# Kernel tuning notes

Hardware: AMD Instinct MI355X
Metric: run time of the kernel (lower is better)

## Reference

```python
import jax, jax.numpy as jnp
import numpy as np

N = 256   # input_size
H = 512   # hidden_size
B = 128   # batch


def _make_masks(n, h):
    # Replicates MADE.create_masks with n_hidden=1
    d_in = np.arange(n)
    d_h = np.arange(h) % (n - 1)
    d_out = np.arange(n) % n - 1  # = arange(n) - 1
    m0 = (d_h[:, None] >= d_in[None, :]).astype(np.float32)   # (H, N)
    m1 = (d_h[:, None] >= d_h[None, :]).astype(np.float32)    # (H, H)
    m2 = (d_out[:, None] >= d_h[None, :]).astype(np.float32)  # (N, H)
    m2 = np.tile(m2, (2, 1))                                   # (2N, H)
    return jnp.asarray(m0), jnp.asarray(m1), jnp.asarray(m2)


def setup_inputs() -> dict:
    key = jax.random.key(0)
    ks = jax.random.split(key, 7)
    s = 0.02
    return {
        "z": jax.random.normal(ks[0], (B, N), jnp.float32),
        "w0": jax.random.normal(ks[1], (H, N), jnp.float32) * s,
        "b0": jax.random.normal(ks[2], (H,), jnp.float32) * s,
        "w1": jax.random.normal(ks[3], (H, H), jnp.float32) * s,
        "b1": jax.random.normal(ks[4], (H,), jnp.float32) * s,
        "w2": jax.random.normal(ks[5], (2 * N, H), jnp.float32) * s,
        "b2": jax.random.normal(ks[6], (2 * N,), jnp.float32) * s,
    }


def reference(z, w0, b0, w1, b1, w2, b2):
    m0, m1, m2 = _make_masks(N, H)
    mw0 = m0 * w0
    mw1 = m1 * w1
    mw2 = m2 * w2

    def net(x):
        h = jax.nn.relu(x @ mw0.T + b0)
        h = jax.nn.relu(h @ mw1.T + b1)
        return h @ mw2.T + b2  # (B, 2N)

    def step(carry, i):
        x, log_det = carry
        out = net(x)
        mu = out[:, i]          # (B,)
        alpha = out[:, N + i]   # (B,)
        x = x.at[:, i].set(mu + z[:, i] * jnp.exp(alpha))
        return (x, log_det + alpha), None

    x0 = jnp.zeros_like(z)
    ld0 = jnp.zeros((z.shape[0],), z.dtype)
    (x, log_det), _ = jax.lax.scan(step, (x0, ld0), jnp.arange(N))
    return x, -log_det
```

## Files before the change

### kernel.cpp

```cpp
#include <hip/hip_runtime.h>

#define NN 256
#define HH 512
#define BB 128
#define PKS (5 * HH)

typedef float f32x4 __attribute__((ext_vector_type(4)));

__global__ __launch_bounds__(512)
void made_prep(const float* __restrict__ w0,
               const float* __restrict__ w1,
               const float* __restrict__ w2,
               float* __restrict__ pk) {
    const int i = blockIdx.x;
    const int k = threadIdx.x;
    const int lev = k % 255;
    float* row = pk + (size_t)i * PKS;
    row[k]          = (lev < i)  ? w2[i * HH + k]        : 0.f;
    row[HH + k]     = (lev < i)  ? w2[(NN + i) * HH + k] : 0.f;
    row[2*HH + k]   = (lev >= i) ? w0[k * NN + i]        : 0.f;
    const int l1 = i % 255;
    row[3*HH + k]   = (lev >= l1) ? w1[k * HH + i]       : 0.f;
    const int j2 = i + 255;
    const int l2 = j2 % 255;
    row[4*HH + k]   = (lev >= l2) ? w1[k * HH + j2]      : 0.f;
}

struct B10 { f32x4 q0,q1,q2,q3,q4,q5,q6,q7,q8,q9; };

__device__ __forceinline__ float rl_f(float v, int lane) {
    return __int_as_float(__builtin_amdgcn_readlane(__float_as_int(v), lane));
}

__device__ __forceinline__ f32x4 ld4(const float* p) { return *(const f32x4*)p; }

__device__ __forceinline__ float q45c(const B10& b, int s) {
    switch (s) {
        case 0: return b.q4[0]; case 1: return b.q4[1];
        case 2: return b.q4[2]; case 3: return b.q4[3];
        case 4: return b.q5[0]; case 5: return b.q5[1];
        case 6: return b.q5[2]; default: return b.q5[3];
    }
}

#define DPP_ADD(v, ctrl, rm) \
    ((v) + __int_as_float(__builtin_amdgcn_update_dpp(0, __float_as_int(v), (ctrl), (rm), 0xf, false)))

__device__ __forceinline__ void reduce2(float& pm, float& pa) {
    pm = DPP_ADD(pm, 0x111, 0xf);  pa = DPP_ADD(pa, 0x111, 0xf);
    pm = DPP_ADD(pm, 0x112, 0xf);  pa = DPP_ADD(pa, 0x112, 0xf);
    pm = DPP_ADD(pm, 0x114, 0xf);  pa = DPP_ADD(pa, 0x114, 0xf);
    pm = DPP_ADD(pm, 0x118, 0xf);  pa = DPP_ADD(pa, 0x118, 0xf);
    pm = DPP_ADD(pm, 0x142, 0xa);  pa = DPP_ADD(pa, 0x142, 0xa);
    pm = DPP_ADD(pm, 0x143, 0xc);  pa = DPP_ADD(pa, 0x143, 0xc);
}

#define DOT8(res, A, B)  do {                                   \
    float t01_ = fmaf(h_[1], (A)[1], h_[0] * (A)[0]);           \
    float t23_ = fmaf(h_[3], (A)[3], h_[2] * (A)[2]);           \
    float t45_ = fmaf(h_[5], (B)[1], h_[4] * (B)[0]);           \
    float t67_ = fmaf(h_[7], (B)[3], h_[6] * (B)[2]);           \
    res = (t01_ + t23_) + (t45_ + t67_);                        \
} while (0)

#define STEP(g, r, BUF) do {                                                 \
    const int i_ = ((g) << 3) | (r);                                         \
    float h_[8];                                                             \
    h_[0] = fmaxf(a1v[0], 0.f); h_[1] = fmaxf(a1v[1], 0.f);                  \
    h_[2] = fmaxf(a1v[2], 0.f); h_[3] = fmaxf(a1v[3], 0.f);                  \
    h_[4] = fmaxf(a1v[4], 0.f); h_[5] = fmaxf(a1v[5], 0.f);                  \
    h_[6] = fmaxf(a1v[6], 0.f); h_[7] = fmaxf(a1v[7], 0.f);                  \
    float pm_, pa_;                                                          \
    DOT8(pa_, BUF.q2, BUF.q3);                                               \
    DOT8(pm_, BUF.q0, BUF.q1);                                               \
    reduce2(pm_, pa_);                                                       \
    const int sB_ = ((r) + 7) & 7;                                           \
    const int LB_ = ((r) == 0) ? ((g) + 31) : ((g) + 32);                    \
    const int zl_ = ((g) << 1) + ((r) >> 2);                                 \
    float a0A_ = rl_f(a0v[(r)], (g));                                        \
    float w0A_ = rl_f(q45c(BUF, (r)), (g));                                  \
    float a0B_ = rl_f(a0v[sB_], LB_);                                        \
    float w0B_ = rl_f(q45c(BUF, sB_), LB_);                                  \
    float ta_ = rl_f(pa_, 63), tm_ = rl_f(pm_, 63);                          \
    float al_ = ta_ + rl_f(b2v[(r)], (g) + 32);                              \
    float mu_ = tm_ + rl_f(b2v[(r)], (g));                                   \
    ldacc += al_;                                                            \
    float zi_ = rl_f(zrv[(r) & 3], zl_);                                     \
    float xi_ = fmaf(zi_, __expf(al_), mu_);                                 \
    xo[(r) & 3] = (t == zl_) ? xi_ : xo[(r) & 3];                            \
    float h0a_ = fmaxf(fmaf(xi_, w0A_, a0A_), 0.f);                          \
    float h0b_ = fmaxf(fmaf(xi_, w0B_, a0B_), 0.f);                          \
    if ((r) < 2 && (g) == 0) {          \
        float a0C_ = rl_f(a0v[6 + (r)], 63);                                 \
        float w0C_ = rl_f(q45c(BUF, 6 + (r)), 63);                           \
        float h0c_ = fmaxf(fmaf(xi_, w0C_, a0C_), 0.f);                      \
        const float* wc_ = ((r) == 0) ? w1c0v : w1c1v;                       \
        a1v[0] = fmaf(h0c_, wc_[0], a1v[0]); a1v[1] = fmaf(h0c_, wc_[1], a1v[1]); \
        a1v[2] = fmaf(h0c_, wc_[2], a1v[2]); a1v[3] = fmaf(h0c_, wc_[3], a1v[3]); \
        a1v[4] = fmaf(h0c_, wc_[4], a1v[4]); a1v[5] = fmaf(h0c_, wc_[5], a1v[5]); \
        a1v[6] = fmaf(h0c_, wc_[6], a1v[6]); a1v[7] = fmaf(h0c_, wc_[7], a1v[7]); \
    }                                                                        \
    a0v[0] = fmaf(xi_, BUF.q4[0], a0v[0]); a0v[1] = fmaf(xi_, BUF.q4[1], a0v[1]); \
    a0v[2] = fmaf(xi_, BUF.q4[2], a0v[2]); a0v[3] = fmaf(xi_, BUF.q4[3], a0v[3]); \
    a0v[4] = fmaf(xi_, BUF.q5[0], a0v[4]); a0v[5] = fmaf(xi_, BUF.q5[1], a0v[5]); \
    a0v[6] = fmaf(xi_, BUF.q5[2], a0v[6]); a0v[7] = fmaf(xi_, BUF.q5[3], a0v[7]); \
    a1v[0] = fmaf(h0b_, BUF.q8[0], fmaf(h0a_, BUF.q6[0], a1v[0]));           \
    a1v[1] = fmaf(h0b_, BUF.q8[1], fmaf(h0a_, BUF.q6[1], a1v[1]));           \
    a1v[2] = fmaf(h0b_, BUF.q8[2], fmaf(h0a_, BUF.q6[2], a1v[2]));           \
    a1v[3] = fmaf(h0b_, BUF.q8[3], fmaf(h0a_, BUF.q6[3], a1v[3]));           \
    a1v[4] = fmaf(h0b_, BUF.q9[0], fmaf(h0a_, BUF.q7[0], a1v[4]));           \
    a1v[5] = fmaf(h0b_, BUF.q9[1], fmaf(h0a_, BUF.q7[1], a1v[5]));           \
    a1v[6] = fmaf(h0b_, BUF.q9[2], fmaf(h0a_, BUF.q7[2], a1v[6]));           \
    a1v[7] = fmaf(h0b_, BUF.q9[3], fmaf(h0a_, BUF.q7[3], a1v[7]));           \
          \
    {                                                                        \
        const float* pf_ = pk + (size_t)((i_ + 4) & 255) * PKS + o8;         \
        BUF.q0 = ld4(pf_);          BUF.q1 = ld4(pf_ + 4);                   \
        BUF.q2 = ld4(pf_ + HH);     BUF.q3 = ld4(pf_ + HH + 4);              \
        BUF.q4 = ld4(pf_ + 2*HH);   BUF.q5 = ld4(pf_ + 2*HH + 4);            \
        BUF.q6 = ld4(pf_ + 3*HH);   BUF.q7 = ld4(pf_ + 3*HH + 4);            \
        BUF.q8 = ld4(pf_ + 4*HH);   BUF.q9 = ld4(pf_ + 4*HH + 4);            \
    }                                                                        \
    __builtin_amdgcn_sched_barrier(0);                                       \
} while (0)

__global__ __launch_bounds__(64, 1)
void made_seq64(const float* __restrict__ z,
                const float* __restrict__ b0g,
                const float* __restrict__ b1g,
                const float* __restrict__ b2g,
                const float* __restrict__ w1,
                const float* __restrict__ pk,
                float* __restrict__ out) {
    const int bb = blockIdx.x;
    const int t  = threadIdx.x;
    const int o8 = t << 3;

    float a0v[8], a1v[8], b2v[8];
    {
        f32x4 a = ld4(b0g + o8), b = ld4(b0g + o8 + 4);
        a0v[0]=a[0]; a0v[1]=a[1]; a0v[2]=a[2]; a0v[3]=a[3];
        a0v[4]=b[0]; a0v[5]=b[1]; a0v[6]=b[2]; a0v[7]=b[3];
        a = ld4(b1g + o8); b = ld4(b1g + o8 + 4);
        a1v[0]=a[0]; a1v[1]=a[1]; a1v[2]=a[2]; a1v[3]=a[3];
        a1v[4]=b[0]; a1v[5]=b[1]; a1v[6]=b[2]; a1v[7]=b[3];
        a = ld4(b2g + o8); b = ld4(b2g + o8 + 4);
        b2v[0]=a[0]; b2v[1]=a[1]; b2v[2]=a[2]; b2v[3]=a[3];
        b2v[4]=b[0]; b2v[5]=b[1]; b2v[6]=b[2]; b2v[7]=b[3];
    }
    float w1c0v[8], w1c1v[8];
    #pragma unroll
    for (int j = 0; j < 8; ++j) {
        const int k = o8 + j;
        w1c0v[j] = w1[k * HH + 510];
        w1c1v[j] = ((k % 255) >= 1) ? w1[k * HH + 511] : 0.f;
    }
    f32x4 z4 = ld4(z + (bb << 8) + (t << 2));
    float zrv[4] = {z4[0], z4[1], z4[2], z4[3]};
    float xo[4]  = {0.f, 0.f, 0.f, 0.f};
    float ldacc  = 0.f;

    B10 Ba, Bb, Bc, Bd;
    {
        const float* p0 = pk + o8;
        Ba.q0 = ld4(p0);        Ba.q1 = ld4(p0 + 4);
        Ba.q2 = ld4(p0 + HH);   Ba.q3 = ld4(p0 + HH + 4);
        Ba.q4 = ld4(p0 + 2*HH); Ba.q5 = ld4(p0 + 2*HH + 4);
        Ba.q6 = ld4(p0 + 3*HH); Ba.q7 = ld4(p0 + 3*HH + 4);
        Ba.q8 = ld4(p0 + 4*HH); Ba.q9 = ld4(p0 + 4*HH + 4);
        const float* p1 = pk + PKS + o8;
        Bb.q0 = ld4(p1);        Bb.q1 = ld4(p1 + 4);
        Bb.q2 = ld4(p1 + HH);   Bb.q3 = ld4(p1 + HH + 4);
        Bb.q4 = ld4(p1 + 2*HH); Bb.q5 = ld4(p1 + 2*HH + 4);
        Bb.q6 = ld4(p1 + 3*HH); Bb.q7 = ld4(p1 + 3*HH + 4);
        Bb.q8 = ld4(p1 + 4*HH); Bb.q9 = ld4(p1 + 4*HH + 4);
        const float* p2 = pk + 2*PKS + o8;
        Bc.q0 = ld4(p2);        Bc.q1 = ld4(p2 + 4);
        Bc.q2 = ld4(p2 + HH);   Bc.q3 = ld4(p2 + HH + 4);
        Bc.q4 = ld4(p2 + 2*HH); Bc.q5 = ld4(p2 + 2*HH + 4);
        Bc.q6 = ld4(p2 + 3*HH); Bc.q7 = ld4(p2 + 3*HH + 4);
        Bc.q8 = ld4(p2 + 4*HH); Bc.q9 = ld4(p2 + 4*HH + 4);
        const float* p3 = pk + 3*PKS + o8;
        Bd.q0 = ld4(p3);        Bd.q1 = ld4(p3 + 4);
        Bd.q2 = ld4(p3 + HH);   Bd.q3 = ld4(p3 + HH + 4);
        Bd.q4 = ld4(p3 + 2*HH); Bd.q5 = ld4(p3 + 2*HH + 4);
        Bd.q6 = ld4(p3 + 3*HH); Bd.q7 = ld4(p3 + 3*HH + 4);
        Bd.q8 = ld4(p3 + 4*HH); Bd.q9 = ld4(p3 + 4*HH + 4);
    }
    __builtin_amdgcn_sched_barrier(0);

    for (int g = 0; g < 32; ++g) {
        STEP(g, 0, Ba); STEP(g, 1, Bb); STEP(g, 2, Bc); STEP(g, 3, Bd);
        STEP(g, 4, Ba); STEP(g, 5, Bb); STEP(g, 6, Bc); STEP(g, 7, Bd);
    }

    *(f32x4*)(out + (bb << 8) + (t << 2)) = (f32x4){xo[0], xo[1], xo[2], xo[3]};
    if (t == 0) out[BB * NN + bb] = -ldacc;
}

__global__ __launch_bounds__(256)
void made_seq_fb(const float* __restrict__ z,
                 const float* __restrict__ w0, const float* __restrict__ b0,
                 const float* __restrict__ w1, const float* __restrict__ b1,
                 const float* __restrict__ w2, const float* __restrict__ b2,
                 float* __restrict__ out) {
    const int bb = blockIdx.x;
    const int t  = threadIdx.x;
    const int u0 = t, u1 = t + 256;
    const int l0 = u0 % 255, s0 = u0 / 255;
    const int l1 = u1 % 255, s1 = u1 / 255;
    const int wave = t >> 6, lane = t & 63;

    __shared__ float red[2][4][2];
    __shared__ float pub[2][3][2];

    float a0_0 = b0[u0], a0_1 = b0[u1];
    float a1_0 = b1[u0], a1_1 = b1[u1];
    float ld = 0.f;

    for (int i = 0; i < NN; ++i) {
        float cw2m0 = (l0 < i) ? w2[i * HH + u0] : 0.f;
        float cw2a0 = (l0 < i) ? w2[(NN + i) * HH + u0] : 0.f;
        float cw2m1 = (l1 < i) ? w2[i * HH + u1] : 0.f;
        float cw2a1 = (l1 < i) ? w2[(NN + i) * HH + u1] : 0.f;
        float cw00  = (l0 >= i) ? w0[u0 * NN + i] : 0.f;
        float cw01  = (l1 >= i) ? w0[u1 * NN + i] : 0.f;
        bool g0 = (l0 >= (i % 255)), g1 = (l1 >= (i % 255));
        float w1a0 = g0 ? w1[u0 * HH + i] : 0.f;
        float w1a1 = g1 ? w1[u1 * HH + i] : 0.f;
        float w1b0 = g0 ? w1[u0 * HH + i + 255] : 0.f;
        float w1b1 = g1 ? w1[u1 * HH + i + 255] : 0.f;

        float h10 = fmaxf(a1_0, 0.f), h11 = fmaxf(a1_1, 0.f);
        float pm = h10 * cw2m0 + h11 * cw2m1;
        float pa = h10 * cw2a0 + h11 * cw2a1;
        #pragma unroll
        for (int offs = 32; offs > 0; offs >>= 1) {
            pm += __shfl_xor(pm, offs);
            pa += __shfl_xor(pa, offs);
        }
        const int bf = i & 1;
        if (lane == 0) { red[bf][wave][0] = pm; red[bf][wave][1] = pa; }
        if (l0 == i) { pub[bf][s0][0] = a0_0; pub[bf][s0][1] = cw00; }
        if (l1 == i) { pub[bf][s1][0] = a0_1; pub[bf][s1][1] = cw01; }
        __syncthreads();

        float mu = b2[i]      + red[bf][0][0] + red[bf][1][0] + red[bf][2][0] + red[bf][3][0];
        float al = b2[NN + i] + red[bf][0][1] + red[bf][1][1] + red[bf][2][1] + red[bf][3][1];
        ld += al;
        float xi = fmaf(z[bb * NN + i], __expf(al), mu);
        if (t == 0) out[bb * NN + i] = xi;

        a0_0 = fmaf(xi, cw00, a0_0);
        a0_1 = fmaf(xi, cw01, a0_1);

        float h0a = fmaxf(fmaf(xi, pub[bf][0][1], pub[bf][0][0]), 0.f);
        float h0b = fmaxf(fmaf(xi, pub[bf][1][1], pub[bf][1][0]), 0.f);
        a1_0 = fmaf(h0a, w1a0, a1_0);
        a1_1 = fmaf(h0a, w1a1, a1_1);
        a1_0 = fmaf(h0b, w1b0, a1_0);
        a1_1 = fmaf(h0b, w1b1, a1_1);
        if (i < 2) {
            float w1c0 = (l0 >= i) ? w1[u0 * HH + i + 510] : 0.f;
            float w1c1 = (l1 >= i) ? w1[u1 * HH + i + 510] : 0.f;
            float h0c = fmaxf(fmaf(xi, pub[bf][2][1], pub[bf][2][0]), 0.f);
            a1_0 = fmaf(h0c, w1c0, a1_0);
            a1_1 = fmaf(h0c, w1c1, a1_1);
        }
        __syncthreads();
    }

    if (t == 0) out[BB * NN + bb] = -ld;
}

extern "C" void kernel_launch(void* const* d_in, const int* in_sizes, int n_in,
                              void* d_out, int out_size, void* d_ws, size_t ws_size,
                              hipStream_t stream) {
    const float* z  = (const float*)d_in[0];
    const float* w0 = (const float*)d_in[1];
    const float* b0 = (const float*)d_in[2];
    const float* w1 = (const float*)d_in[3];
    const float* b1 = (const float*)d_in[4];
    const float* w2 = (const float*)d_in[5];
    const float* b2 = (const float*)d_in[6];
    float* out = (float*)d_out;

    const size_t need = (size_t)NN * PKS * sizeof(float);
    if (ws_size >= need) {
        float* pk = (float*)d_ws;
        made_prep<<<NN, 512, 0, stream>>>(w0, w1, w2, pk);
        made_seq64<<<BB, 64, 0, stream>>>(z, b0, b1, b2, w1, pk, out);
    } else {
        made_seq_fb<<<BB, 256, 0, stream>>>(z, w0, b0, w1, b1, w2, b2, out);
    }
}
```

Before: 83.79 us.

## Process two batch rows per wavefront to reuse prefetched weight buffers

Each 64-lane block now handles two batch elements, so every weight tile loaded from the packed workspace feeds two dependency chains instead of one, and the grid is halved. The paired mu/alpha reduction is also restructured: a cross-half shuffle lets each half-wave reduce one quantity, which saves one DPP step. Interleaving two independent chains can hide the latency of the serial per-step chain, but it doubles accumulator registers and per-step ALU work per wave, and only half as many CUs are busy.

```diff
diff --git a/kernel.cpp b/kernel.cpp
--- a/kernel.cpp
+++ b/kernel.cpp
@@ -3,6 +3,7 @@
 #define NN 256
 #define HH 512
 #define BB 128
+#define EPW 2
 #define PKS (5 * HH)
 
 typedef float f32x4 __attribute__((ext_vector_type(4)));
@@ -42,17 +43,28 @@
         case 6: return b.q5[2]; default: return b.q5[3];
     }
 }
+__device__ __forceinline__ float q67c(const B10& b, int j) {
+    return (j < 4) ? b.q6[j] : b.q7[j - 4];
+}
+__device__ __forceinline__ float q89c(const B10& b, int j) {
+    return (j < 4) ? b.q8[j] : b.q9[j - 4];
+}
 
 #define DPP_ADD(v, ctrl, rm) \
     ((v) + __int_as_float(__builtin_amdgcn_update_dpp(0, __float_as_int(v), (ctrl), (rm), 0xf, false)))
 
-__device__ __forceinline__ void reduce2(float& pm, float& pa) {
-    pm = DPP_ADD(pm, 0x111, 0xf);  pa = DPP_ADD(pa, 0x111, 0xf);
-    pm = DPP_ADD(pm, 0x112, 0xf);  pa = DPP_ADD(pa, 0x112, 0xf);
-    pm = DPP_ADD(pm, 0x114, 0xf);  pa = DPP_ADD(pa, 0x114, 0xf);
-    pm = DPP_ADD(pm, 0x118, 0xf);  pa = DPP_ADD(pa, 0x118, 0xf);
-    pm = DPP_ADD(pm, 0x142, 0xa);  pa = DPP_ADD(pa, 0x142, 0xa);
-    pm = DPP_ADD(pm, 0x143, 0xc);  pa = DPP_ADD(pa, 0x143, 0xc);
+__device__ __forceinline__ void reduce_half(float pm, float pa, int t,
+                                            float& tm, float& ta) {
+    float c = (t < 32) ? pm : pa;
+    float d = (t < 32) ? pa : pm;
+    c += __shfl_xor(d, 32);
+    c = DPP_ADD(c, 0x111, 0xf);
+    c = DPP_ADD(c, 0x112, 0xf);
+    c = DPP_ADD(c, 0x114, 0xf);
+    c = DPP_ADD(c, 0x118, 0xf);
+    c = DPP_ADD(c, 0x142, 0xa);
+    tm = rl_f(c, 31);
+    ta = rl_f(c, 63);
 }
 
 #define DOT8(res, A, B)  do {                                   \
@@ -64,54 +76,51 @@
 } while (0)
 
 #define STEP(g, r, BUF) do {                                                 \
-    const int i_ = ((g) << 3) | (r);                                         \
-    float h_[8];                                                             \
-    h_[0] = fmaxf(a1v[0], 0.f); h_[1] = fmaxf(a1v[1], 0.f);                  \
-    h_[2] = fmaxf(a1v[2], 0.f); h_[3] = fmaxf(a1v[3], 0.f);                  \
-    h_[4] = fmaxf(a1v[4], 0.f); h_[5] = fmaxf(a1v[5], 0.f);                  \
-    h_[6] = fmaxf(a1v[6], 0.f); h_[7] = fmaxf(a1v[7], 0.f);                  \
-    float pm_, pa_;                                                          \
-    DOT8(pa_, BUF.q2, BUF.q3);                                               \
-    DOT8(pm_, BUF.q0, BUF.q1);                                               \
-    reduce2(pm_, pa_);                                                       \
+    const int i_  = ((g) << 3) | (r);                                        \
     const int sB_ = ((r) + 7) & 7;                                           \
     const int LB_ = ((r) == 0) ? ((g) + 31) : ((g) + 32);                    \
     const int zl_ = ((g) << 1) + ((r) >> 2);                                 \
-    float a0A_ = rl_f(a0v[(r)], (g));                                        \
-    float w0A_ = rl_f(q45c(BUF, (r)), (g));                                  \
-    float a0B_ = rl_f(a0v[sB_], LB_);                                        \
-    float w0B_ = rl_f(q45c(BUF, sB_), LB_);                                  \
-    float ta_ = rl_f(pa_, 63), tm_ = rl_f(pm_, 63);                          \
-    float al_ = ta_ + rl_f(b2v[(r)], (g) + 32);                              \
-    float mu_ = tm_ + rl_f(b2v[(r)], (g));                                   \
-    ldacc += al_;                                                            \
-    float zi_ = rl_f(zrv[(r) & 3], zl_);                                     \
-    float xi_ = fmaf(zi_, __expf(al_), mu_);                                 \
-    xo[(r) & 3] = (t == zl_) ? xi_ : xo[(r) & 3];                            \
-    float h0a_ = fmaxf(fmaf(xi_, w0A_, a0A_), 0.f);                          \
-    float h0b_ = fmaxf(fmaf(xi_, w0B_, a0B_), 0.f);                          \
-    if ((r) < 2 && (g) == 0) {          \
-        float a0C_ = rl_f(a0v[6 + (r)], 63);                                 \
-        float w0C_ = rl_f(q45c(BUF, 6 + (r)), 63);                           \
-        float h0c_ = fmaxf(fmaf(xi_, w0C_, a0C_), 0.f);                      \
-        const float* wc_ = ((r) == 0) ? w1c0v : w1c1v;                       \
-        a1v[0] = fmaf(h0c_, wc_[0], a1v[0]); a1v[1] = fmaf(h0c_, wc_[1], a1v[1]); \
-        a1v[2] = fmaf(h0c_, wc_[2], a1v[2]); a1v[3] = fmaf(h0c_, wc_[3], a1v[3]); \
-        a1v[4] = fmaf(h0c_, wc_[4], a1v[4]); a1v[5] = fmaf(h0c_, wc_[5], a1v[5]); \
-        a1v[6] = fmaf(h0c_, wc_[6], a1v[6]); a1v[7] = fmaf(h0c_, wc_[7], a1v[7]); \
+    const float w0A_ = rl_f(q45c(BUF, (r)), (g));                            \
+    const float w0B_ = rl_f(q45c(BUF, sB_), LB_);                            \
+    const float b2m_ = rl_f(b2v[(r)], (g));                                  \
+    const float b2a_ = rl_f(b2v[(r)], (g) + 32);                             \
+    _Pragma("unroll")                                                        \
+    for (int e = 0; e < EPW; ++e) {                                          \
+        float h_[8];                                                         \
+        _Pragma("unroll")                                                    \
+        for (int j = 0; j < 8; ++j) h_[j] = fmaxf(a1v[e][j], 0.f);           \
+        float pm_, pa_;                                                      \
+        DOT8(pa_, BUF.q2, BUF.q3);                                           \
+        DOT8(pm_, BUF.q0, BUF.q1);                                           \
+        float tm_, ta_;                                                      \
+        reduce_half(pm_, pa_, t, tm_, ta_);                                  \
+        float mu_ = tm_ + b2m_;                                              \
+        float al_ = ta_ + b2a_;                                              \
+        ldacc[e] += al_;                                                     \
+        float zi_ = rl_f(zrv[e][(r) & 3], zl_);                              \
+        float xi_ = fmaf(zi_, __expf(al_), mu_);                             \
+        xo[e][(r) & 3] = (t == zl_) ? xi_ : xo[e][(r) & 3];                  \
+        float a0A_ = rl_f(a0v[e][(r)], (g));                                 \
+        float a0B_ = rl_f(a0v[e][sB_], LB_);                                 \
+        float h0a_ = fmaxf(fmaf(xi_, w0A_, a0A_), 0.f);                      \
+        float h0b_ = fmaxf(fmaf(xi_, w0B_, a0B_), 0.f);                      \
+        if ((r) < 2 && (g) == 0) {      \
+            float a0C_ = rl_f(a0v[e][6 + (r)], 63);                          \
+            float w0C_ = rl_f(q45c(BUF, 6 + (r)), 63);                       \
+            float h0c_ = fmaxf(fmaf(xi_, w0C_, a0C_), 0.f);                  \
+            const float* wc_ = ((r) == 0) ? w1c0v : w1c1v;                   \
+            _Pragma("unroll")                                                \
+            for (int j = 0; j < 8; ++j)                                      \
+                a1v[e][j] = fmaf(h0c_, wc_[j], a1v[e][j]);                   \
+        }                                                                    \
+        _Pragma("unroll")                                                    \
+        for (int j = 0; j < 8; ++j)                                          \
+            a0v[e][j] = fmaf(xi_, q45c(BUF, j), a0v[e][j]);                  \
+        _Pragma("unroll")                                                    \
+        for (int j = 0; j < 8; ++j)                                          \
+            a1v[e][j] = fmaf(h0b_, q89c(BUF, j),                             \
+                             fmaf(h0a_, q67c(BUF, j), a1v[e][j]));           \
     }                                                                        \
-    a0v[0] = fmaf(xi_, BUF.q4[0], a0v[0]); a0v[1] = fmaf(xi_, BUF.q4[1], a0v[1]); \
-    a0v[2] = fmaf(xi_, BUF.q4[2], a0v[2]); a0v[3] = fmaf(xi_, BUF.q4[3], a0v[3]); \
-    a0v[4] = fmaf(xi_, BUF.q5[0], a0v[4]); a0v[5] = fmaf(xi_, BUF.q5[1], a0v[5]); \
-    a0v[6] = fmaf(xi_, BUF.q5[2], a0v[6]); a0v[7] = fmaf(xi_, BUF.q5[3], a0v[7]); \
-    a1v[0] = fmaf(h0b_, BUF.q8[0], fmaf(h0a_, BUF.q6[0], a1v[0]));           \
-    a1v[1] = fmaf(h0b_, BUF.q8[1], fmaf(h0a_, BUF.q6[1], a1v[1]));           \
-    a1v[2] = fmaf(h0b_, BUF.q8[2], fmaf(h0a_, BUF.q6[2], a1v[2]));           \
-    a1v[3] = fmaf(h0b_, BUF.q8[3], fmaf(h0a_, BUF.q6[3], a1v[3]));           \
-    a1v[4] = fmaf(h0b_, BUF.q9[0], fmaf(h0a_, BUF.q7[0], a1v[4]));           \
-    a1v[5] = fmaf(h0b_, BUF.q9[1], fmaf(h0a_, BUF.q7[1], a1v[5]));           \
-    a1v[6] = fmaf(h0b_, BUF.q9[2], fmaf(h0a_, BUF.q7[2], a1v[6]));           \
-    a1v[7] = fmaf(h0b_, BUF.q9[3], fmaf(h0a_, BUF.q7[3], a1v[7]));           \
           \
     {                                                                        \
         const float* pf_ = pk + (size_t)((i_ + 4) & 255) * PKS + o8;         \
@@ -136,29 +145,33 @@
     const int t  = threadIdx.x;
     const int o8 = t << 3;
 
-    float a0v[8], a1v[8], b2v[8];
+    float a0v[EPW][8], a1v[EPW][8], zrv[EPW][4], xo[EPW][4], ldacc[EPW];
+    float b2v[8], w1c0v[8], w1c1v[8];
     {
         f32x4 a = ld4(b0g + o8), b = ld4(b0g + o8 + 4);
-        a0v[0]=a[0]; a0v[1]=a[1]; a0v[2]=a[2]; a0v[3]=a[3];
-        a0v[4]=b[0]; a0v[5]=b[1]; a0v[6]=b[2]; a0v[7]=b[3];
-        a = ld4(b1g + o8); b = ld4(b1g + o8 + 4);
-        a1v[0]=a[0]; a1v[1]=a[1]; a1v[2]=a[2]; a1v[3]=a[3];
-        a1v[4]=b[0]; a1v[5]=b[1]; a1v[6]=b[2]; a1v[7]=b[3];
-        a = ld4(b2g + o8); b = ld4(b2g + o8 + 4);
-        b2v[0]=a[0]; b2v[1]=a[1]; b2v[2]=a[2]; b2v[3]=a[3];
-        b2v[4]=b[0]; b2v[5]=b[1]; b2v[6]=b[2]; b2v[7]=b[3];
-    }
-    float w1c0v[8], w1c1v[8];
+        f32x4 c = ld4(b1g + o8), d = ld4(b1g + o8 + 4);
+        f32x4 e4 = ld4(b2g + o8), f4 = ld4(b2g + o8 + 4);
+        #pragma unroll
+        for (int e = 0; e < EPW; ++e) {
+            #pragma unroll
+            for (int j = 0; j < 4; ++j) {
+                a0v[e][j] = a[j];  a0v[e][4 + j] = b[j];
+                a1v[e][j] = c[j];  a1v[e][4 + j] = d[j];
+            }
+            f32x4 zz = ld4(z + ((size_t)(EPW * bb + e) << 8) + (t << 2));
+            #pragma unroll
+            for (int j = 0; j < 4; ++j) { zrv[e][j] = zz[j]; xo[e][j] = 0.f; }
+            ldacc[e] = 0.f;
+        }
+        #pragma unroll
+        for (int j = 0; j < 4; ++j) { b2v[j] = e4[j]; b2v[4 + j] = f4[j]; }
+    }
     #pragma unroll
     for (int j = 0; j < 8; ++j) {
         const int k = o8 + j;
         w1c0v[j] = w1[k * HH + 510];
         w1c1v[j] = ((k % 255) >= 1) ? w1[k * HH + 511] : 0.f;
     }
-    f32x4 z4 = ld4(z + (bb << 8) + (t << 2));
-    float zrv[4] = {z4[0], z4[1], z4[2], z4[3]};
-    float xo[4]  = {0.f, 0.f, 0.f, 0.f};
-    float ldacc  = 0.f;
 
     B10 Ba, Bb, Bc, Bd;
     {
@@ -194,8 +207,12 @@
         STEP(g, 4, Ba); STEP(g, 5, Bb); STEP(g, 6, Bc); STEP(g, 7, Bd);
     }
 
-    *(f32x4*)(out + (bb << 8) + (t << 2)) = (f32x4){xo[0], xo[1], xo[2], xo[3]};
-    if (t == 0) out[BB * NN + bb] = -ldacc;
+    #pragma unroll
+    for (int e = 0; e < EPW; ++e) {
+        *(f32x4*)(out + ((size_t)(EPW * bb + e) << 8) + (t << 2)) =
+            (f32x4){xo[e][0], xo[e][1], xo[e][2], xo[e][3]};
+        if (t == 0) out[BB * NN + EPW * bb + e] = -ldacc[e];
+    }
 }
 
 __global__ __launch_bounds__(256)
@@ -289,7 +306,7 @@
     if (ws_size >= need) {
         float* pk = (float*)d_ws;
         made_prep<<<NN, 512, 0, stream>>>(w0, w1, w2, pk);
-        made_seq64<<<BB, 64, 0, stream>>>(z, b0, b1, b2, w1, pk, out);
+        made_seq64<<<BB / EPW, 64, 0, stream>>>(z, b0, b1, b2, w1, pk, out);
     } else {
         made_seq_fb<<<BB, 256, 0, stream>>>(z, w0, b0, w1, b1, w2, b2, out);
     }
```

New measurement: 127.1 us. +51.7%, slower.
